# Kernel optimization log

Hardware: AMD Instinct MI355X
Metric: run time of the kernel (lower is better)

## Reference

```python
import jax, jax.numpy as jnp
import numpy as np

B, S, D, H = 4, 2048, 1024, 16
HD = D // H  # head_dim = 64


def setup_inputs() -> dict:
    key = jax.random.key(0)
    ks = jax.random.split(key, 7)
    sc = 0.02
    return {
        "data": jax.random.normal(ks[0], (B, S, D), jnp.float32),
        "context": jax.random.normal(ks[1], (B, S, D), jnp.float32),
        "Wq": jax.random.normal(ks[2], (D, D), jnp.float32) * sc,
        "bq": jnp.zeros((D,), jnp.float32),
        "Wk": jax.random.normal(ks[3], (D, D), jnp.float32) * sc,
        "bk": jnp.zeros((D,), jnp.float32),
        "Wv": jax.random.normal(ks[4], (D, D), jnp.float32) * sc,
        "bv": jnp.zeros((D,), jnp.float32),
        "Wo": jax.random.normal(ks[5], (D, D), jnp.float32) * sc,
        "bo": jnp.zeros((D,), jnp.float32),
    }


def reference(data, context, Wq, bq, Wk, bk, Wv, bv, Wo, bo):
    # Projections (torch Linear: x @ W.T + b; here W stored as [in, out])
    Q = data @ Wq + bq          # [B,S,D]
    K = context @ Wk + bk
    V = context @ Wv + bv
    # split heads -> [B,H,S,HD]
    Q = Q.reshape(B, S, H, HD).transpose(0, 2, 1, 3)
    K = K.reshape(B, S, H, HD).transpose(0, 2, 1, 3)
    V = V.reshape(B, S, H, HD).transpose(0, 2, 1, 3)
    scale = jnp.sqrt(jnp.asarray(HD, Q.dtype))
    scores = jnp.einsum("bhqd,bhkd->bhqk", Q, K) / scale  # [B,H,S,S]
    causal = jnp.tril(jnp.ones((S, S), bool))              # row >= col
    scores = jnp.where(causal[None, None], scores, jnp.asarray(-jnp.inf, scores.dtype))
    probs = jax.nn.softmax(scores, axis=-1)
    Z = jnp.einsum("bhqk,bhkd->bhqd", probs, V)            # [B,H,S,HD]
    Z = Z.transpose(0, 2, 1, 3).reshape(B, S, D)
    return Z @ Wo + bo
```

## Files before the change

### kernel.cpp

```cpp
#include <hip/hip_runtime.h>

#define B_  4
#define S_  2048
#define D_  1024
#define H_  16
#define HD_ 64
#define M_  (B_*S_)

typedef _Float16 f16;
typedef f16  f16x8 __attribute__((ext_vector_type(8)));
typedef f16  f16x4 __attribute__((ext_vector_type(4)));
typedef float f32x4 __attribute__((ext_vector_type(4)));

__device__ __forceinline__ void gload_lds16(const f16* g, f16* l) {
    __builtin_amdgcn_global_load_lds(
        (const __attribute__((address_space(1))) void*)g,
        (__attribute__((address_space(3))) void*)l, 16, 0, 0);
}

__global__ __launch_bounds__(256) void cvt2_kernel(const float* __restrict__ a,
                                                   const float* __restrict__ c,
                                                   f16* __restrict__ out, int n4each) {
    int i = blockIdx.x * 256 + threadIdx.x;
    const float* src = (i < n4each) ? a : c;
    int j = (i < n4each) ? i : i - n4each;
    f32x4 v = *reinterpret_cast<const f32x4*>(src + (size_t)j * 4);
    *reinterpret_cast<f16x4*>(out + (size_t)i * 4) = __builtin_convertvector(v, f16x4);
}

__global__ __launch_bounds__(256) void transpose_cvt4_kernel(const float* __restrict__ Wq,
                                                             const float* __restrict__ Wk,
                                                             const float* __restrict__ Wv,
                                                             const float* __restrict__ Wo,
                                                             f16* __restrict__ WT) {
    __shared__ float tile[32][33];
    const int z = blockIdx.z;
    const float* W = (z == 0) ? Wq : (z == 1) ? Wk : (z == 2) ? Wv : Wo;
    f16* dst = WT + (size_t)z * D_ * D_;
    const int n0 = blockIdx.x * 32, k0 = blockIdx.y * 32;
    const int tx = threadIdx.x & 31, ty = threadIdx.x >> 5;
#pragma unroll
    for (int j = 0; j < 4; ++j)
        tile[ty + 8 * j][tx] = W[(size_t)(k0 + ty + 8 * j) * D_ + n0 + tx];
    __syncthreads();
#pragma unroll
    for (int j = 0; j < 4; ++j)
        dst[(size_t)(n0 + ty + 8 * j) * D_ + k0 + tx] = (f16)tile[tx][ty + 8 * j];
}

template <int MODE>
__global__ __launch_bounds__(256, 2) void gemm3p(const f16* __restrict__ Adata,
                                                 const f16* __restrict__ Actx,
                                                 const f16* __restrict__ Wbase,
                                                 const float* __restrict__ b0,
                                                 const float* __restrict__ b1,
                                                 const float* __restrict__ b2,
                                                 f16* __restrict__ Qb,
                                                 f16* __restrict__ Kb,
                                                 f16* __restrict__ VtB,
                                                 float* __restrict__ Cout) {
    extern __shared__ __align__(16) f16 SM[];
    constexpr int K = D_;
    constexpr int NT = K / 32;
    const int id = (int)blockIdx.x;
    const int seg = (MODE == 0) ? (id >> 8) : 0;
    const int sid = (MODE == 0) ? (id & 255) : id;
    const int work = (sid & 7) * 32 + (sid >> 3);
    const int wy = work >> 2, wx = work & 3;
    const f16* __restrict__ A = (MODE == 0) ? (seg ? Actx : Adata) : Adata;
    const f16* __restrict__ Wt = Wbase + (size_t)seg * D_ * D_;
    const int m0 = wy * 128, n0 = wx * 256;
    const int tid = (int)threadIdx.x;
    const int w = tid >> 6, lr = tid & 15, lg = (tid & 63) >> 4;
    const int wr = w >> 1, wc = w & 1;
    const int sw = (lr >> 1) & 3;

    auto stage = [&](int buf, int kt) {
        const int kk0 = kt * 32;
        f16* base = SM + buf * 12288;
#pragma unroll
        for (int j = 0; j < 2; ++j) {
            const int c = j * 256 + tid;
            const int row = c >> 2;
            const int ks = ((c & 3) ^ ((row >> 1) & 3)) * 8;
            gload_lds16(A + (size_t)(m0 + row) * K + kk0 + ks,
                        base + (j * 256 + w * 64) * 8);
        }
#pragma unroll
        for (int j = 0; j < 4; ++j) {
            const int c = j * 256 + tid;
            const int row = c >> 2;
            const int ks = ((c & 3) ^ ((row >> 1) & 3)) * 8;
            gload_lds16(Wt + (size_t)(n0 + row) * K + kk0 + ks,
                        base + 4096 + (j * 256 + w * 64) * 8);
        }
    };
    auto LDA = [&](int buf, int m) -> f16x8 {
        return *reinterpret_cast<const f16x8*>(
            SM + buf * 12288 + (wr * 64 + m * 16 + lr) * 32 + ((lg ^ sw) * 8));
    };
    auto LDB = [&](int buf, int n) -> f16x8 {
        return *reinterpret_cast<const f16x8*>(
            SM + buf * 12288 + 4096 + (wc * 128 + n * 16 + lr) * 32 + ((lg ^ sw) * 8));
    };

    f32x4 acc[4][8] = {};
    stage(0, 0);
    stage(1, 1);
    asm volatile("s_waitcnt vmcnt(6)" ::: "memory");
    __builtin_amdgcn_s_barrier();

    int buf = 0;
    for (int t = 0; t < NT; ++t) {
        if (t + 2 < NT) {
            int nb = buf + 2; if (nb >= 3) nb -= 3;
            stage(nb, t + 2);
        }
        f16x8 a[4], b[8];
#pragma unroll
        for (int m = 0; m < 4; ++m) a[m] = LDA(buf, m);
#pragma unroll
        for (int n = 0; n < 8; ++n) b[n] = LDB(buf, n);
        __builtin_amdgcn_s_setprio(1);
#pragma unroll
        for (int m = 0; m < 4; ++m)
#pragma unroll
            for (int n = 0; n < 8; ++n)
                acc[m][n] = __builtin_amdgcn_mfma_f32_16x16x32_f16(a[m], b[n], acc[m][n], 0, 0, 0);
        __builtin_amdgcn_s_setprio(0);
        if (t + 2 < NT) {
            asm volatile("s_waitcnt vmcnt(6)" ::: "memory");
        } else if (t + 1 < NT) {
            asm volatile("s_waitcnt vmcnt(0)" ::: "memory");
        }
        __builtin_amdgcn_s_barrier();
        if (++buf >= 3) buf = 0;
    }
    if (MODE == 1) {
#pragma unroll
        for (int n = 0; n < 8; ++n) {
            const int col = n0 + wc * 128 + n * 16 + lr;
            const float bvv = b0[col];
#pragma unroll
            for (int m = 0; m < 4; ++m) {
                const int row = m0 + wr * 64 + m * 16 + lg * 4;
#pragma unroll
                for (int r = 0; r < 4; ++r)
                    Cout[(size_t)(row + r) * D_ + col] = acc[m][n][r] + bvv;
            }
        }
    } else {
        const float* bias = (seg == 0) ? b0 : (seg == 1) ? b1 : b2;
#pragma unroll
        for (int n = 0; n < 8; ++n) {
            const int lc = n0 + wc * 128 + n * 16 + lr;
            const float bvv = bias[lc];
#pragma unroll
            for (int m = 0; m < 4; ++m) {
                const int row = m0 + wr * 64 + m * 16 + lg * 4;
                if (seg == 2) {
                    const int bb = row >> 11, s0 = row & 2047;
                    f16x4 v;
#pragma unroll
                    for (int r = 0; r < 4; ++r) v[r] = (f16)(acc[m][n][r] + bvv);
                    *reinterpret_cast<f16x4*>(VtB + ((size_t)(bb * D_ + lc)) * S_ + s0) = v;
                } else {
                    f16* dst = seg ? Kb : Qb;
#pragma unroll
                    for (int r = 0; r < 4; ++r)
                        dst[(size_t)(row + r) * D_ + lc] = (f16)(acc[m][n][r] + bvv);
                }
            }
        }
    }
}

__global__ __launch_bounds__(256, 2) void attn_kernel(const f16* __restrict__ Q,
                                                      const f16* __restrict__ Kg,
                                                      const f16* __restrict__ Vt,
                                                      f16* __restrict__ Z) {
    __shared__ __align__(16) f16 KL[2][64 * 64];
    __shared__ __align__(16) f16 VL[2][64 * 64];
    __shared__ __align__(16) f16 Pl[4][32][72];
    const int h = blockIdx.x, b = blockIdx.y, pp = blockIdx.z;
    const int tid = threadIdx.x, w = tid >> 6, l = tid & 63, lr = l & 15, lg = l >> 4;
    const size_t base   = ((size_t)b * S_) * D_ + h * HD_;
    const size_t vtbase = ((size_t)(b * D_ + h * HD_)) * S_;
    const f16* __restrict__ Kbase = Kg + base;
    const f16* __restrict__ Vbase = Vt + vtbase;
    const float sc = 0.125f * 1.44269504f;
    const int sw_xor = lr & 7;
    f16x8 onesv;
#pragma unroll
    for (int i = 0; i < 8; ++i) onesv[i] = (f16)1.0f;

    auto stageKV = [&](int buf, int t0) {
#pragma unroll
        for (int i = 0; i < 2; ++i) {
            const int c = i * 256 + tid;
            const int row = c >> 3, g16 = (c & 7) ^ (row & 7);
            f16* dstK = &KL[buf][(i * 256 + w * 64) * 8];
            f16* dstV = &VL[buf][(i * 256 + w * 64) * 8];
            gload_lds16(Kbase + (size_t)(t0 + row) * D_ + g16 * 8, dstK);
            gload_lds16(Vbase + (size_t)row * S_ + t0 + g16 * 8, dstV);
        }
    };

    for (int half = 0; half < 2; ++half) {
        const int qt = half ? pp : (15 - pp);
        const int q0 = qt * 128, wq0 = q0 + w * 32;
        const int ntw = ((wq0 + 31) >> 6) + 1;
        const int ntb = qt * 2 + 2;

        f16x8 qf[2][2];
#pragma unroll
        for (int mf = 0; mf < 2; ++mf)
#pragma unroll
            for (int kd = 0; kd < 2; ++kd)
                qf[mf][kd] = *reinterpret_cast<const f16x8*>(
                    Q + base + (size_t)(wq0 + mf * 16 + lr) * D_ + kd * 32 + lg * 8);

        f32x4 zacc[2][4] = {};
        f32x4 lsv[2] = {};
        float mrun[2] = {-3.0e38f, -3.0e38f};

        stageKV(0, 0);
        for (int t = 0; t < ntb; ++t) {
            const int buf = t & 1;
            if (t + 1 < ntb) {
                stageKV(buf ^ 1, (t + 1) * 64);
                asm volatile("s_waitcnt vmcnt(4)" ::: "memory");
            } else {
                asm volatile("s_waitcnt vmcnt(0)" ::: "memory");
            }
            __builtin_amdgcn_s_barrier();
            if (t < ntw) {
                const int t0 = t * 64;
                f16x8 kf[2][4];
#pragma unroll
                for (int kd = 0; kd < 2; ++kd)
#pragma unroll
                    for (int n = 0; n < 4; ++n)
                        kf[kd][n] = *reinterpret_cast<const f16x8*>(
                            &KL[buf][(n * 16 + lr) * 64 + (((kd * 4 + lg) ^ sw_xor) * 8)]);
                f32x4 sf[2][4] = {};
                __builtin_amdgcn_s_setprio(1);
#pragma unroll
                for (int kd = 0; kd < 2; ++kd)
#pragma unroll
                    for (int n = 0; n < 4; ++n)
#pragma unroll
                        for (int mf = 0; mf < 2; ++mf)
                            sf[mf][n] = __builtin_amdgcn_mfma_f32_16x16x32_f16(kf[kd][n], qf[mf][kd], sf[mf][n], 0, 0, 0);
                __builtin_amdgcn_s_setprio(0);
                f16x8 vf[2][4];
#pragma unroll
                for (int kt = 0; kt < 2; ++kt)
#pragma unroll
                    for (int n = 0; n < 4; ++n)
                        vf[kt][n] = *reinterpret_cast<const f16x8*>(
                            &VL[buf][(n * 16 + lr) * 64 + (((kt * 4 + lg) ^ sw_xor) * 8)]);
                if (t == ntw - 1) {
#pragma unroll
                    for (int mf = 0; mf < 2; ++mf)
#pragma unroll
                        for (int n = 0; n < 4; ++n)
#pragma unroll
                            for (int r = 0; r < 4; ++r)
                                if ((t0 + n * 16 + lg * 4 + r) > (wq0 + mf * 16 + lr))
                                    sf[mf][n][r] = -3.0e38f;
                }
#pragma unroll
                for (int mf = 0; mf < 2; ++mf) {
                    f32x4 t4;
#pragma unroll
                    for (int r = 0; r < 4; ++r)
                        t4[r] = fmaxf(fmaxf(sf[mf][0][r], sf[mf][1][r]), fmaxf(sf[mf][2][r], sf[mf][3][r]));
                    float vmax = fmaxf(fmaxf(t4[0], t4[1]), fmaxf(t4[2], t4[3]));
                    vmax = fmaxf(vmax, __shfl_xor(vmax, 16));
                    vmax = fmaxf(vmax, __shfl_xor(vmax, 32));
                    const float vs = vmax * sc;
                    const bool norm = !__all(vs <= mrun[mf] + 10.0f);
                    if (norm) {
                        const float mnew = fmaxf(mrun[mf], vs);
                        const float al = __builtin_amdgcn_exp2f(mrun[mf] - mnew);
                        mrun[mf] = mnew;
#pragma unroll
                        for (int r = 0; r < 4; ++r) {
                            const float ar = __shfl(al, lg * 4 + r);
#pragma unroll
                            for (int n = 0; n < 4; ++n) zacc[mf][n][r] *= ar;
                            lsv[mf][r] *= ar;
                        }
                    }
#pragma unroll
                    for (int n = 0; n < 4; ++n) {
                        f32x4 p;
#pragma unroll
                        for (int r = 0; r < 4; ++r)
                            p[r] = __builtin_amdgcn_exp2f(fmaf(sf[mf][n][r], sc, -mrun[mf]));
                        f16x4 pv;
#pragma unroll
                        for (int r = 0; r < 4; ++r) pv[r] = (f16)p[r];
                        *reinterpret_cast<f16x4*>(&Pl[w][mf * 16 + lr][n * 16 + lg * 4]) = pv;
                    }
                }
#pragma unroll
                for (int kt = 0; kt < 2; ++kt) {
                    f16x8 pa[2];
#pragma unroll
                    for (int mf = 0; mf < 2; ++mf)
                        pa[mf] = *reinterpret_cast<const f16x8*>(&Pl[w][mf * 16 + lr][kt * 32 + lg * 8]);
                    __builtin_amdgcn_s_setprio(1);
#pragma unroll
                    for (int n = 0; n < 4; ++n)
#pragma unroll
                        for (int mf = 0; mf < 2; ++mf)
                            zacc[mf][n] = __builtin_amdgcn_mfma_f32_16x16x32_f16(pa[mf], vf[kt][n], zacc[mf][n], 0, 0, 0);
#pragma unroll
                    for (int mf = 0; mf < 2; ++mf)
                        lsv[mf] = __builtin_amdgcn_mfma_f32_16x16x32_f16(pa[mf], onesv, lsv[mf], 0, 0, 0);
                    __builtin_amdgcn_s_setprio(0);
                }
            }
            __builtin_amdgcn_s_barrier();
        }
#pragma unroll
        for (int mf = 0; mf < 2; ++mf) {
            f32x4 inv;
#pragma unroll
            for (int r = 0; r < 4; ++r) inv[r] = 1.0f / lsv[mf][r];
#pragma unroll
            for (int r = 0; r < 4; ++r)
#pragma unroll
                for (int n = 0; n < 4; ++n)
                    Z[base + (size_t)(wq0 + mf * 16 + lg * 4 + r) * D_ + n * 16 + lr] =
                        (f16)(zacc[mf][n][r] * inv[r]);
        }
    }
}

extern "C" void kernel_launch(void* const* d_in, const int* in_sizes, int n_in,
                              void* d_out, int out_size, void* d_ws, size_t ws_size,
                              hipStream_t stream) {
    const float* data    = (const float*)d_in[0];
    const float* context = (const float*)d_in[1];
    const float* Wq = (const float*)d_in[2];
    const float* bq = (const float*)d_in[3];
    const float* Wk = (const float*)d_in[4];
    const float* bk = (const float*)d_in[5];
    const float* Wv = (const float*)d_in[6];
    const float* bv = (const float*)d_in[7];
    const float* Wo = (const float*)d_in[8];
    const float* bo = (const float*)d_in[9];

    const size_t MD = (size_t)M_ * D_;
    const size_t DD = (size_t)D_ * D_;
    f16* dataB = (f16*)d_ws;
    f16* ctxB  = dataB + MD;
    f16* WqT   = ctxB + MD;
    f16* WkT   = WqT + DD;
    f16* WvT   = WkT + DD;
    f16* WoT   = WvT + DD;
    f16* Qb    = WoT + DD;
    f16* Kb    = Qb + MD;
    f16* VtB   = Kb + MD;
    f16* Zb    = VtB + MD;

    (void)WkT; (void)WvT;

    const int n4 = (int)(MD / 4);
    cvt2_kernel<<<2 * n4 / 256, 256, 0, stream>>>(data, context, dataB, n4);
    transpose_cvt4_kernel<<<dim3(32, 32, 4), 256, 0, stream>>>(Wq, Wk, Wv, Wo, WqT);

    (void)hipFuncSetAttribute(reinterpret_cast<const void*>(gemm3p<0>),
                              hipFuncAttributeMaxDynamicSharedMemorySize, 73728);
    (void)hipFuncSetAttribute(reinterpret_cast<const void*>(gemm3p<1>),
                              hipFuncAttributeMaxDynamicSharedMemorySize, 73728);

    gemm3p<0><<<768, 256, 73728, stream>>>(dataB, ctxB, WqT, bq, bk, bv,
                                           Qb, Kb, VtB, nullptr);

    attn_kernel<<<dim3(H_, B_, 8), 256, 0, stream>>>(Qb, Kb, VtB, Zb);

    gemm3p<1><<<256, 256, 73728, stream>>>(Zb, nullptr, WoT, bo, nullptr, nullptr,
                                           nullptr, nullptr, nullptr, (float*)d_out);
}
```

Baseline: 169.2 us.

## Fuse fp32-to-fp16 activation conversion into QKV projection GEMM A-loads

Removes the separate conversion kernel for data/context and has the QKV GEMM load fp32 activations into registers, convert them to fp16, and write them swizzled into LDS, while weights still stream via direct global-to-LDS loads. This avoids writing and re-reading a full fp16 copy of both activation tensors. In exchange the GEMM reads twice the A bytes per tile, uses more registers for the staged A data, and adds an extra LDS write and wait in each pipeline step. The output projection GEMM is split into its own non-templated kernel.

New measurement: 167.1 us. Within noise of the previous version (-1.3%).

```diff
diff --git a/kernel.cpp b/kernel.cpp
--- a/kernel.cpp
+++ b/kernel.cpp
@@ -16,16 +16,6 @@
     __builtin_amdgcn_global_load_lds(
         (const __attribute__((address_space(1))) void*)g,
         (__attribute__((address_space(3))) void*)l, 16, 0, 0);
-}
-
-__global__ __launch_bounds__(256) void cvt2_kernel(const float* __restrict__ a,
-                                                   const float* __restrict__ c,
-                                                   f16* __restrict__ out, int n4each) {
-    int i = blockIdx.x * 256 + threadIdx.x;
-    const float* src = (i < n4each) ? a : c;
-    int j = (i < n4each) ? i : i - n4each;
-    f32x4 v = *reinterpret_cast<const f32x4*>(src + (size_t)j * 4);
-    *reinterpret_cast<f16x4*>(out + (size_t)i * 4) = __builtin_convertvector(v, f16x4);
 }
 
 __global__ __launch_bounds__(256) void transpose_cvt4_kernel(const float* __restrict__ Wq,
@@ -48,27 +38,157 @@
         dst[(size_t)(n0 + ty + 8 * j) * D_ + k0 + tx] = (f16)tile[tx][ty + 8 * j];
 }
 
-template <int MODE>
-__global__ __launch_bounds__(256, 2) void gemm3p(const f16* __restrict__ Adata,
-                                                 const f16* __restrict__ Actx,
-                                                 const f16* __restrict__ Wbase,
-                                                 const float* __restrict__ b0,
-                                                 const float* __restrict__ b1,
-                                                 const float* __restrict__ b2,
-                                                 f16* __restrict__ Qb,
-                                                 f16* __restrict__ Kb,
-                                                 f16* __restrict__ VtB,
-                                                 float* __restrict__ Cout) {
+__global__ __launch_bounds__(256, 2) void gemm_qkvf(const float* __restrict__ Fa,
+                                                    const float* __restrict__ Fc,
+                                                    const f16* __restrict__ Wbase,
+                                                    const float* __restrict__ b0,
+                                                    const float* __restrict__ b1,
+                                                    const float* __restrict__ b2,
+                                                    f16* __restrict__ Qb,
+                                                    f16* __restrict__ Kb,
+                                                    f16* __restrict__ VtB) {
     extern __shared__ __align__(16) f16 SM[];
     constexpr int K = D_;
     constexpr int NT = K / 32;
     const int id = (int)blockIdx.x;
-    const int seg = (MODE == 0) ? (id >> 8) : 0;
-    const int sid = (MODE == 0) ? (id & 255) : id;
+    const int seg = id >> 8;
+    const int sid = id & 255;
     const int work = (sid & 7) * 32 + (sid >> 3);
     const int wy = work >> 2, wx = work & 3;
-    const f16* __restrict__ A = (MODE == 0) ? (seg ? Actx : Adata) : Adata;
+    const float* __restrict__ Af = seg ? Fc : Fa;
     const f16* __restrict__ Wt = Wbase + (size_t)seg * D_ * D_;
+    const int m0 = wy * 128, n0 = wx * 256;
+    const int tid = (int)threadIdx.x;
+    const int w = tid >> 6, lr = tid & 15, lg = (tid & 63) >> 4;
+    const int wr = w >> 1, wc = w & 1;
+    const int sw = (lr >> 1) & 3;
+    const int arow = tid >> 1;
+    const int s0g = (2 * (tid & 1)) ^ ((arow >> 1) & 3);
+    const int s1g = s0g ^ 1;
+    const float* __restrict__ Abase = Af + (size_t)(m0 + arow) * K;
+
+    auto stageB = [&](int buf, int kt) {
+        const int kk0 = kt * 32;
+#pragma unroll
+        for (int j = 0; j < 4; ++j) {
+            const int c = j * 256 + tid;
+            const int row = c >> 2;
+            const int ks = ((c & 3) ^ ((row >> 1) & 3)) * 8;
+            gload_lds16(Wt + (size_t)(n0 + row) * K + kk0 + ks,
+                        SM + buf * 12288 + 4096 + (j * 256 + w * 64) * 8);
+        }
+    };
+    auto LDA = [&](int buf, int m) -> f16x8 {
+        return *reinterpret_cast<const f16x8*>(
+            SM + buf * 12288 + (wr * 64 + m * 16 + lr) * 32 + ((lg ^ sw) * 8));
+    };
+    auto LDB = [&](int buf, int n) -> f16x8 {
+        return *reinterpret_cast<const f16x8*>(
+            SM + buf * 12288 + 4096 + (wc * 128 + n * 16 + lr) * 32 + ((lg ^ sw) * 8));
+    };
+
+    f32x4 rA0[4], rA1[4];
+    f32x4 acc[4][8] = {};
+
+#define LOAD_A(RS, KT)                                                          \
+    {                                                                           \
+        const float* ap_ = Abase + (KT) * 32;                                   \
+        RS[0] = *reinterpret_cast<const f32x4*>(ap_ + s0g * 8);                 \
+        RS[1] = *reinterpret_cast<const f32x4*>(ap_ + s0g * 8 + 4);             \
+        RS[2] = *reinterpret_cast<const f32x4*>(ap_ + s1g * 8);                 \
+        RS[3] = *reinterpret_cast<const f32x4*>(ap_ + s1g * 8 + 4);             \
+    }
+#define WRITE_A(RS, BUF)                                                        \
+    {                                                                           \
+        f16* ad_ = SM + (BUF) * 12288 + tid * 16;                               \
+        *reinterpret_cast<f16x8*>(ad_) = __builtin_shufflevector(               \
+            __builtin_convertvector(RS[0], f16x4),                              \
+            __builtin_convertvector(RS[1], f16x4), 0, 1, 2, 3, 4, 5, 6, 7);     \
+        *reinterpret_cast<f16x8*>(ad_ + 8) = __builtin_shufflevector(           \
+            __builtin_convertvector(RS[2], f16x4),                              \
+            __builtin_convertvector(RS[3], f16x4), 0, 1, 2, 3, 4, 5, 6, 7);     \
+    }
+#define TILE_BODY(T, RISS, RWR)                                                 \
+    {                                                                           \
+        const int buf_ = (T) % 3;                                               \
+        if ((T) + 2 < NT) {                                                     \
+            LOAD_A(RISS, (T) + 2);                                              \
+            stageB(((T) + 2) % 3, (T) + 2);                                     \
+            asm volatile("" ::: "memory");                                      \
+        }                                                                       \
+        f16x8 a_[4], b_[8];                                                     \
+        _Pragma("unroll") for (int m = 0; m < 4; ++m) a_[m] = LDA(buf_, m);     \
+        _Pragma("unroll") for (int n = 0; n < 8; ++n) b_[n] = LDB(buf_, n);     \
+        __builtin_amdgcn_s_setprio(1);                                          \
+        _Pragma("unroll") for (int m = 0; m < 4; ++m)                           \
+            _Pragma("unroll") for (int n = 0; n < 8; ++n)                       \
+                acc[m][n] = __builtin_amdgcn_mfma_f32_16x16x32_f16(             \
+                    a_[m], b_[n], acc[m][n], 0, 0, 0);                          \
+        __builtin_amdgcn_s_setprio(0);                                          \
+        if ((T) + 1 < NT) {                                                     \
+            if ((T) + 2 < NT) { asm volatile("s_waitcnt vmcnt(8)" ::: "memory"); } \
+            else              { asm volatile("s_waitcnt vmcnt(0)" ::: "memory"); } \
+            WRITE_A(RWR, ((T) + 1) % 3);                                        \
+            asm volatile("s_waitcnt lgkmcnt(0)" ::: "memory");                  \
+            __builtin_amdgcn_s_barrier();                                       \
+        }                                                                       \
+    }
+
+    LOAD_A(rA0, 0);
+    stageB(0, 0);
+    asm volatile("" ::: "memory");
+    LOAD_A(rA1, 1);
+    stageB(1, 1);
+    asm volatile("s_waitcnt vmcnt(8)" ::: "memory");
+    WRITE_A(rA0, 0);
+    asm volatile("s_waitcnt lgkmcnt(0)" ::: "memory");
+    __builtin_amdgcn_s_barrier();
+
+    int t = 0;
+    for (; t < NT - 2; t += 2) {
+        TILE_BODY(t,     rA0, rA1);
+        TILE_BODY(t + 1, rA1, rA0);
+    }
+    TILE_BODY(NT - 2, rA0, rA1);
+    TILE_BODY(NT - 1, rA1, rA0);
+#undef TILE_BODY
+#undef WRITE_A
+#undef LOAD_A
+
+    const float* bias = (seg == 0) ? b0 : (seg == 1) ? b1 : b2;
+#pragma unroll
+    for (int n = 0; n < 8; ++n) {
+        const int lc = n0 + wc * 128 + n * 16 + lr;
+        const float bvv = bias[lc];
+#pragma unroll
+        for (int m = 0; m < 4; ++m) {
+            const int row = m0 + wr * 64 + m * 16 + lg * 4;
+            if (seg == 2) {
+                const int bb = row >> 11, s0 = row & 2047;
+                f16x4 v;
+#pragma unroll
+                for (int r = 0; r < 4; ++r) v[r] = (f16)(acc[m][n][r] + bvv);
+                *reinterpret_cast<f16x4*>(VtB + ((size_t)(bb * D_ + lc)) * S_ + s0) = v;
+            } else {
+                f16* dst = seg ? Kb : Qb;
+#pragma unroll
+                for (int r = 0; r < 4; ++r)
+                    dst[(size_t)(row + r) * D_ + lc] = (f16)(acc[m][n][r] + bvv);
+            }
+        }
+    }
+}
+
+__global__ __launch_bounds__(256, 2) void gemm_out3(const f16* __restrict__ A,
+                                                    const f16* __restrict__ Wt,
+                                                    const float* __restrict__ bias,
+                                                    float* __restrict__ Cout) {
+    extern __shared__ __align__(16) f16 SM[];
+    constexpr int K = D_;
+    constexpr int NT = K / 32;
+    const int id = (int)blockIdx.x;
+    const int work = (id & 7) * 32 + (id >> 3);
+    const int wy = work >> 2, wx = work & 3;
     const int m0 = wy * 128, n0 = wx * 256;
     const int tid = (int)threadIdx.x;
     const int w = tid >> 6, lr = tid & 15, lg = (tid & 63) >> 4;
@@ -136,41 +256,16 @@
         __builtin_amdgcn_s_barrier();
         if (++buf >= 3) buf = 0;
     }
-    if (MODE == 1) {
-#pragma unroll
-        for (int n = 0; n < 8; ++n) {
-            const int col = n0 + wc * 128 + n * 16 + lr;
-            const float bvv = b0[col];
-#pragma unroll
-            for (int m = 0; m < 4; ++m) {
-                const int row = m0 + wr * 64 + m * 16 + lg * 4;
-#pragma unroll
-                for (int r = 0; r < 4; ++r)
-                    Cout[(size_t)(row + r) * D_ + col] = acc[m][n][r] + bvv;
-            }
-        }
-    } else {
-        const float* bias = (seg == 0) ? b0 : (seg == 1) ? b1 : b2;
-#pragma unroll
-        for (int n = 0; n < 8; ++n) {
-            const int lc = n0 + wc * 128 + n * 16 + lr;
-            const float bvv = bias[lc];
-#pragma unroll
-            for (int m = 0; m < 4; ++m) {
-                const int row = m0 + wr * 64 + m * 16 + lg * 4;
-                if (seg == 2) {
-                    const int bb = row >> 11, s0 = row & 2047;
-                    f16x4 v;
-#pragma unroll
-                    for (int r = 0; r < 4; ++r) v[r] = (f16)(acc[m][n][r] + bvv);
-                    *reinterpret_cast<f16x4*>(VtB + ((size_t)(bb * D_ + lc)) * S_ + s0) = v;
-                } else {
-                    f16* dst = seg ? Kb : Qb;
-#pragma unroll
-                    for (int r = 0; r < 4; ++r)
-                        dst[(size_t)(row + r) * D_ + lc] = (f16)(acc[m][n][r] + bvv);
-                }
-            }
+#pragma unroll
+    for (int n = 0; n < 8; ++n) {
+        const int col = n0 + wc * 128 + n * 16 + lr;
+        const float bvv = bias[col];
+#pragma unroll
+        for (int m = 0; m < 4; ++m) {
+            const int row = m0 + wr * 64 + m * 16 + lg * 4;
+#pragma unroll
+            for (int r = 0; r < 4; ++r)
+                Cout[(size_t)(row + r) * D_ + col] = acc[m][n][r] + bvv;
         }
     }
 }
@@ -356,33 +451,24 @@
 
     const size_t MD = (size_t)M_ * D_;
     const size_t DD = (size_t)D_ * D_;
-    f16* dataB = (f16*)d_ws;
-    f16* ctxB  = dataB + MD;
-    f16* WqT   = ctxB + MD;
-    f16* WkT   = WqT + DD;
-    f16* WvT   = WkT + DD;
-    f16* WoT   = WvT + DD;
-    f16* Qb    = WoT + DD;
+    f16* WqT   = (f16*)d_ws;
+    f16* WoT   = WqT + 3 * DD;
+    f16* Qb    = WqT + 4 * DD;
     f16* Kb    = Qb + MD;
     f16* VtB   = Kb + MD;
     f16* Zb    = VtB + MD;
 
-    (void)WkT; (void)WvT;
-
-    const int n4 = (int)(MD / 4);
-    cvt2_kernel<<<2 * n4 / 256, 256, 0, stream>>>(data, context, dataB, n4);
     transpose_cvt4_kernel<<<dim3(32, 32, 4), 256, 0, stream>>>(Wq, Wk, Wv, Wo, WqT);
 
-    (void)hipFuncSetAttribute(reinterpret_cast<const void*>(gemm3p<0>),
+    (void)hipFuncSetAttribute(reinterpret_cast<const void*>(gemm_qkvf),
                               hipFuncAttributeMaxDynamicSharedMemorySize, 73728);
-    (void)hipFuncSetAttribute(reinterpret_cast<const void*>(gemm3p<1>),
+    (void)hipFuncSetAttribute(reinterpret_cast<const void*>(gemm_out3),
                               hipFuncAttributeMaxDynamicSharedMemorySize, 73728);
 
-    gemm3p<0><<<768, 256, 73728, stream>>>(dataB, ctxB, WqT, bq, bk, bv,
-                                           Qb, Kb, VtB, nullptr);
+    gemm_qkvf<<<768, 256, 73728, stream>>>(data, context, WqT, bq, bk, bv,
+                                           Qb, Kb, VtB);
 
     attn_kernel<<<dim3(H_, B_, 8), 256, 0, stream>>>(Qb, Kb, VtB, Zb);
 
-    gemm3p<1><<<256, 256, 73728, stream>>>(Zb, nullptr, WoT, bo, nullptr, nullptr,
-                                           nullptr, nullptr, nullptr, (float*)d_out);
-}
+    gemm_out3<<<256, 256, 73728, stream>>>(Zb, WoT, bo, (float*)d_out);
+}
```
